# Optimization experiments

Measured on AMD Instinct MI355X. Metric: run time of the kernel, lower is better.

Reference implementation:

```python
import jax, jax.numpy as jnp
import numpy as np
from jax import lax

G, BS = 8, 32  # group_num, blocksize


def conv(x, w, b=None, stride=1, pad=0):
    out = lax.conv_general_dilated(x, w, (stride, stride), [(pad, pad), (pad, pad)],
                                   dimension_numbers=('NCHW', 'OIHW', 'NCHW'))
    if b is not None:
        out = out + b[None, :, None, None]
    return out


def prelu(x, a):
    return jnp.where(x >= 0, x, a * x)


def reshape_adap(x, bs):
    # faithful vectorized form of My_Reshape_Adap: channel c = co*bs*bs + p*bs + q
    # goes to output[b, co, i*bs+p, j*bs+q]
    B, C, h, w = x.shape
    co = C // (bs * bs)
    return x.reshape(B, co, bs, bs, h, w).transpose(0, 1, 4, 2, 5, 3).reshape(B, co, h * bs, w * bs)


def setup_inputs() -> dict:
    key = jax.random.key(0)
    ks = jax.random.split(key, 24)
    rn = lambda k, shp, s: (jax.random.normal(k, shp, dtype=jnp.float32) * s)
    inp = {
        'x': rn(ks[0], (1, 1, 256, 256), 1.0),
        'sample_w': rn(ks[1], (G, 13, 1, 32, 32), 0.03),
        'up_w': rn(ks[2], (G, 1024, 13, 1, 1), 0.2),
        'up_b': rn(ks[3], (G, 1024), 0.02),
        'h1_w': rn(ks[4], (G, 64, 1, 3, 3), 0.2),
        'h1_b': rn(ks[5], (G, 64), 0.02),
        'h1_a': jnp.full((G,), 0.25, jnp.float32),
        'fus_w': rn(ks[6], (G - 1, 64, 128, 3, 3), 0.03),
        'fus_b': rn(ks[7], (G - 1, 64), 0.02),
        'fus_a': jnp.full((G - 1,), 0.25, jnp.float32),
        't2_w': rn(ks[8], (G, 64, 64, 3, 3), 0.04),
        't2_b': rn(ks[9], (G, 64), 0.02),
        't2_a': jnp.full((G,), 0.25, jnp.float32),
        't3_w': rn(ks[10], (G, 64, 64, 3, 3), 0.04),
        't3_b': rn(ks[11], (G, 64), 0.02),
        't3_a': jnp.full((G,), 0.25, jnp.float32),
        't4_w': rn(ks[12], (G, 64, 64, 3, 3), 0.04),
        't4_b': rn(ks[13], (G, 64), 0.02),
        't4_a': jnp.full((G,), 0.25, jnp.float32),
        't5_w': rn(ks[14], (G, 1, 64, 3, 3), 0.04),
        't5_b': rn(ks[15], (G, 1), 0.02),
    }
    return inp


def reference(x, sample_w, up_w, up_b, h1_w, h1_b, h1_a, fus_w, fus_b, fus_a,
              t2_w, t2_b, t2_a, t3_w, t3_b, t3_a, t4_w, t4_b, t4_a, t5_w, t5_b):
    outs = []
    feature = None
    for m in range(G):
        # SamplingModule: conv(1->13, k=32, s=32, no bias)
        s = conv(x, sample_w[m], stride=BS)
        # HeadBlock: 1x1 upsample (13->1024) + block scatter reshape + conv(1->64)+PReLU
        u = conv(s, up_w[m], up_b[m])
        r = reshape_adap(u, BS)                       # [B,1,H,W]
        h = prelu(conv(r, h1_w[m], h1_b[m], pad=1), h1_a[m])  # [B,64,H,W]
        if m == 0:
            feature = h
        else:
            # Fusion_concate: conv(128->64)+PReLU on channel concat
            cat = jnp.concatenate([feature, h], axis=1)
            feature = prelu(conv(cat, fus_w[m - 1], fus_b[m - 1], pad=1), fus_a[m - 1])
        t = prelu(conv(feature, t2_w[m], t2_b[m], pad=1), t2_a[m])
        t = prelu(conv(t, t3_w[m], t3_b[m], pad=1), t3_a[m])
        t = prelu(conv(t, t4_w[m], t4_b[m], pad=1), t4_a[m])
        outs.append(conv(t, t5_w[m], t5_b[m], pad=1))
    return jnp.stack(outs)  # [G, B, 1, H, W]
```

## Files before the change

kernel.cpp:

```cpp
#include <hip/hip_runtime.h>

constexpr int H = 256, W = 256, NPIX = H * W;
constexpr int PW = 258;
constexpr size_t PLANE = (size_t)PW * PW * 64;

typedef _Float16 half8 __attribute__((ext_vector_type(8)));
typedef _Float16 half4 __attribute__((ext_vector_type(4)));
typedef float    f32x4 __attribute__((ext_vector_type(4)));
typedef float    f32x16 __attribute__((ext_vector_type(16)));

__device__ __forceinline__ void gl16(const _Float16* g, _Float16* l)
{
    __builtin_amdgcn_global_load_lds(
        (const __attribute__((address_space(1))) unsigned int*)g,
        (__attribute__((address_space(3))) unsigned int*)l, 16, 0, 0);
}

__global__ __launch_bounds__(256)
void prep_k(const float* __restrict__ x, const float* __restrict__ sw,
            const float* __restrict__ uw, const float* __restrict__ ub,
            const float* __restrict__ t2w, const float* __restrict__ t3w,
            const float* __restrict__ t4w, const float* __restrict__ fusw,
            _Float16* __restrict__ planes, _Float16* __restrict__ w16,
            float* __restrict__ r_all)
{
    const int b = blockIdx.x, t = threadIdx.x;
    for (int idx = b * 256 + t; idx < 24 * 1028 * 8; idx += 512 * 256) {
        int c = idx & 7, rem = idx >> 3;
        int p = rem / 1028, bb = rem % 1028;
        int gy, gx;
        if (bb < 258)      { gy = 0;            gx = bb; }
        else if (bb < 516) { gy = 257;          gx = bb - 258; }
        else if (bb < 772) { gy = bb - 516 + 1; gx = 0; }
        else               { gy = bb - 772 + 1; gx = 257; }
        f32x4 z = {0.f, 0.f, 0.f, 0.f};
        *(f32x4*)(planes + (size_t)p * PLANE + ((size_t)(gy * PW + gx) * 64) + c * 8) = z;
    }
    for (int idx = b * 256 + t; idx < 38 * 36864; idx += 512 * 256) {
        int blk = idx / 36864, r2 = idx % 36864;
        int e = r2 & 7, co = (r2 >> 3) & 63, hh = (r2 >> 9) & 1, kk = (r2 >> 10) & 3,
            tap = r2 >> 12;
        const float* src; int cin, cib;
        if (blk < 24) {
            int which = blk >> 3, m = blk & 7;
            src = (which == 0 ? t2w : which == 1 ? t3w : t4w) + (size_t)m * 64 * 64 * 9;
            cin = 64; cib = 0;
        } else {
            int f = (blk - 24) >> 1; cib = ((blk - 24) & 1) * 64;
            src = fusw + (size_t)f * 64 * 128 * 9; cin = 128;
        }
        int ci = cib + (kk * 2 + hh) * 8 + e;
        w16[idx] = (_Float16)src[((size_t)co * cin + ci) * 9 + tap];
    }
    {
        int m = b >> 6, ij = b & 63;
        int i = ij >> 3, j = ij & 7;
        __shared__ float s_lds[16];
        if (t < 208) {
            int c = t >> 4, sub = t & 15;
            float acc = 0.f;
            for (int k = sub * 64; k < sub * 64 + 64; ++k) {
                int p = k >> 5, q = k & 31;
                acc += x[(i * 32 + p) * W + (j * 32 + q)] * sw[(m * 13 + c) * 1024 + k];
            }
            #pragma unroll
            for (int off = 8; off; off >>= 1) acc += __shfl_down(acc, off, 16);
            if (sub == 0) s_lds[c] = acc;
        }
        __syncthreads();
        const float* uwm = uw + m * 1024 * 13;
        float* rm = r_all + m * NPIX;
        #pragma unroll
        for (int pi = 0; pi < 4; ++pi) {
            int px = pi * 256 + t;
            int p = px >> 5, q = px & 31;
            int oc = p * 32 + q;
            float acc = ub[m * 1024 + oc];
            #pragma unroll
            for (int c = 0; c < 13; ++c) acc = fmaf(uwm[oc * 13 + c], s_lds[c], acc);
            rm[((i * 32 + p) << 8) + j * 32 + q] = acc;
        }
    }
}

__global__ __launch_bounds__(256, 2)
void conv_mfma_k(const _Float16* __restrict__ in0, const _Float16* __restrict__ w0,
                 const float* __restrict__ bias, const float* __restrict__ alpha,
                 _Float16* __restrict__ out)
{
    const int t    = threadIdx.x;
    const int lane = t & 63;
    const int wv   = t >> 6;
    const int b    = blockIdx.x;
    const int m    = b >> 6;
    const int rem  = b & 63;
    const int xh   = rem & 1;
    const int y0   = (rem >> 1) << 3;

    const _Float16* inp0 = in0 + (size_t)m * PLANE;
    _Float16*       outp = out + (size_t)m * PLANE;
    const _Float16* wp0  = w0 + (size_t)m * 36864;
    const float*    bp   = bias + m * 64;
    const float     slope = alpha[m];
    const int x0 = xh << 7;

    const int h = lane >> 5, cl = lane & 31;
    const int px0 = (wv & 1) * 64, cobase = (wv >> 1) * 32;

    extern __shared__ __align__(16) char smem[];
    _Float16* li = (_Float16*)smem;

    half8 Areg[36];
    #pragma unroll
    for (int tap = 0; tap < 9; ++tap)
        #pragma unroll
        for (int kk = 0; kk < 4; ++kk)
            Areg[tap*4+kk] = *(const half8*)(wp0 +
                (size_t)(((tap*4+kk)*2 + h)*64 + cobase + cl) * 8);

    auto stage_row = [&](int pr) {
        const int slot = pr & 3;
        #pragma unroll
        for (int i = 0; i < 5; ++i) {
            int f = i * 256 + t;
            if (i < 4 || f < 1040) {
                int hx = f >> 3, c = f & 7;
                gl16(inp0 + ((size_t)(pr * PW + x0 + hx) * 64 + (c ^ (hx & 7)) * 8),
                     li + (size_t)(slot * 1040 + f) * 8);
            }
        }
    };

    f32x16 acc0, acc1;

    stage_row(y0); stage_row(y0 + 1); stage_row(y0 + 2);
    __syncthreads();
    #pragma unroll 1
    for (int s = 0; s < 8; ++s) {
        if (s < 7) stage_row(y0 + s + 3);
        #pragma unroll
        for (int q = 0; q < 4; ++q)
            #pragma unroll
            for (int j = 0; j < 4; ++j) {
                float bb = bp[cobase + q * 8 + 4 * h + j];
                acc0[q*4+j] = bb; acc1[q*4+j] = bb;
            }
        __builtin_amdgcn_s_setprio(1);
        #pragma unroll
        for (int tap = 0; tap < 9; ++tap) {
            const int dy = tap / 3, dx = tap % 3;
            const int slot = (y0 + s + dy) & 3;
            const int hx0 = px0 + cl + dx;
            const int hx1 = hx0 + 32;
            const int sw8 = hx0 & 7;
            #pragma unroll
            for (int kk = 0; kk < 4; ++kk) {
                const int c = kk * 2 + h;
                half8 b0 = *(const half8*)(li + ((size_t)((slot*130 + hx0)*8 + (c ^ sw8))) * 8);
                half8 b1 = *(const half8*)(li + ((size_t)((slot*130 + hx1)*8 + (c ^ sw8))) * 8);
                acc0 = __builtin_amdgcn_mfma_f32_32x32x16_f16(Areg[tap*4+kk], b0, acc0, 0, 0, 0);
                acc1 = __builtin_amdgcn_mfma_f32_32x32x16_f16(Areg[tap*4+kk], b1, acc1, 0, 0, 0);
            }
        }
        __builtin_amdgcn_s_setprio(0);
        const int y = y0 + s;
        #pragma unroll
        for (int pt = 0; pt < 2; ++pt) {
            const size_t gp = (size_t)((y + 1) * PW + (x0 + px0 + pt * 32 + cl + 1)) * 64;
            const f32x16& A0 = pt ? acc1 : acc0;
            #pragma unroll
            for (int q = 0; q < 4; ++q) {
                half4 v0;
                #pragma unroll
                for (int j = 0; j < 4; ++j) {
                    float xv = A0[q*4+j];
                    xv = xv >= 0.f ? xv : slope * xv;
                    v0[j] = (_Float16)xv;
                }
                *(half4*)(outp + gp + cobase + q * 8 + 4 * h) = v0;
            }
        }
        if (s < 7) {
            asm volatile("s_waitcnt vmcnt(8)" ::: "memory");
            __builtin_amdgcn_s_barrier();
            __builtin_amdgcn_sched_barrier(0);
        }
    }
}

template <int FIRST>
__global__ __launch_bounds__(256, 2)
void fus_k(const _Float16* __restrict__ fprev, _Float16* __restrict__ f0out,
           const float* __restrict__ rm_prev, const float* __restrict__ rm_cur,
           const float* __restrict__ h1w_prev, const float* __restrict__ h1b_prev,
           const float* __restrict__ h1a_prev,
           const float* __restrict__ h1w_cur, const float* __restrict__ h1b_cur,
           const float* __restrict__ h1a_cur,
           const _Float16* __restrict__ wf, const _Float16* __restrict__ wh,
           const float* __restrict__ bias, const float* __restrict__ alpha,
           _Float16* __restrict__ outp)
{
    const int t = threadIdx.x, lane = t & 63, wv = t >> 6;
    const int b = blockIdx.x;
    const int xcd = b & 7, u = b >> 3, xq = u & 3, band = u >> 2;
    const int y0 = xcd * 32 + band * 2, x0 = xq * 64;
    const int h = lane >> 5, cl = lane & 31;
    const int px0 = (wv & 1) * 32, cobase = (wv >> 1) * 32;

    __shared__ __align__(16) _Float16 ringF[4 * 528 * 8];
    __shared__ __align__(16) _Float16 ringH[4 * 528 * 8];

    auto hcomp = [&](const float* rm, const float* h1w, const float* h1b,
                     float hs, _Float16* ring, _Float16* f0w) {
        const int c8 = t & 7;
        float wreg[72];
        #pragma unroll
        for (int i = 0; i < 18; ++i)
            *(f32x4*)(wreg + i * 4) = *(const f32x4*)(h1w + c8 * 72 + i * 4);
        float b8[8];
        #pragma unroll
        for (int j = 0; j < 8; ++j) b8[j] = h1b[c8 * 8 + j];

        #pragma unroll
        for (int it = 0; it < 9; ++it) {
            int idx = it * 256 + t;
            if (it < 8 || idx < 2112) {
                int pl = idx >> 3;
                int r  = pl / 66, hx = pl - r * 66;
                int gy = y0 - 1 + r, gx = x0 - 1 + hx;
                half8 o = {0,0,0,0,0,0,0,0};
                if ((unsigned)gy < 256u && (unsigned)gx < 256u) {
                    float v[9];
                    #pragma unroll
                    for (int dy = 0; dy < 3; ++dy) {
                        int ry = gy + dy - 1;
                        #pragma unroll
                        for (int dx = 0; dx < 3; ++dx) {
                            int rx = gx + dx - 1;
                            v[dy*3+dx] = ((unsigned)ry < 256u && (unsigned)rx < 256u)
                                       ? rm[(ry << 8) + rx] : 0.f;
                        }
                    }
                    #pragma unroll
                    for (int j = 0; j < 8; ++j) {
                        float av = b8[j];
                        #pragma unroll
                        for (int k = 0; k < 9; ++k) av = fmaf(v[k], wreg[j*9+k], av);
                        av = av >= 0.f ? av : hs * av;
                        o[j] = (_Float16)av;
                    }
                    if (f0w && r >= 1 && r <= 2 && hx >= 1 && hx <= 64)
                        *(half8*)(f0w + ((size_t)((gy + 1) * PW + (gx + 1)) * 64)
                                  + c8 * 8) = o;
                }
                *(half8*)(ring + (size_t)(r * 528 + hx * 8 + (c8 ^ (hx & 7))) * 8) = o;
            }
        }
    };

    if (FIRST) {
        hcomp(rm_prev, h1w_prev, h1b_prev, h1a_prev[0], ringF, f0out);
    } else {
        #pragma unroll
        for (int i = 0; i < 9; ++i) {
            int idx = i * 256 + t;
            if (i < 8 || idx < 2112) {
                int r = idx / 528, f = idx - r * 528;
                int hx = f >> 3, c = f & 7;
                gl16(fprev + ((size_t)((y0 + r) * PW + x0 + hx) * 64 + (c ^ (hx & 7)) * 8),
                     ringF + (size_t)idx * 8);
            }
        }
    }
    hcomp(rm_cur, h1w_cur, h1b_cur, h1a_cur[0], ringH, nullptr);
    __builtin_amdgcn_sched_barrier(0);

    half8 Areg[36];
    auto load_A = [&](const _Float16* w) {
        #pragma unroll
        for (int tap = 0; tap < 9; ++tap)
            #pragma unroll
            for (int kk = 0; kk < 4; ++kk)
                Areg[tap*4+kk] = *(const half8*)(w +
                    (size_t)(((tap*4+kk)*2 + h)*64 + cobase + cl) * 8);
    };
    load_A(wf);

    f32x16 acc0, acc1;
    #pragma unroll
    for (int q = 0; q < 4; ++q)
        #pragma unroll
        for (int j = 0; j < 4; ++j) {
            float bb = bias[cobase + q * 8 + 4 * h + j];
            acc0[q*4+j] = bb; acc1[q*4+j] = bb;
        }

    __syncthreads();

    auto cpass = [&](const _Float16* ring) {
        __builtin_amdgcn_s_setprio(1);
        #pragma unroll
        for (int tap = 0; tap < 9; ++tap) {
            const int dy = tap / 3, dx = tap % 3;
            const int hx = px0 + cl + dx;
            const int sw = hx & 7;
            #pragma unroll
            for (int kk = 0; kk < 4; ++kk) {
                const int c = kk * 2 + h;
                half8 b0 = *(const half8*)(ring + ((size_t)(((dy    )*528) + hx*8 + (c ^ sw))) * 8);
                half8 b1 = *(const half8*)(ring + ((size_t)(((dy + 1)*528) + hx*8 + (c ^ sw))) * 8);
                acc0 = __builtin_amdgcn_mfma_f32_32x32x16_f16(Areg[tap*4+kk], b0, acc0, 0, 0, 0);
                acc1 = __builtin_amdgcn_mfma_f32_32x32x16_f16(Areg[tap*4+kk], b1, acc1, 0, 0, 0);
            }
        }
        __builtin_amdgcn_s_setprio(0);
    };

    cpass(ringF);
    load_A(wh);
    cpass(ringH);

    const float slope = alpha[0];
    #pragma unroll
    for (int s = 0; s < 2; ++s) {
        const size_t gp = (size_t)((y0 + s + 1) * PW + (x0 + px0 + cl + 1)) * 64 + cobase;
        const f32x16& A0 = s ? acc1 : acc0;
        #pragma unroll
        for (int q = 0; q < 4; ++q) {
            half4 v;
            #pragma unroll
            for (int j = 0; j < 4; ++j) {
                float xv = A0[q*4+j];
                xv = xv >= 0.f ? xv : slope * xv;
                v[j] = (_Float16)xv;
            }
            *(half4*)(outp + gp + q * 8 + 4 * h) = v;
        }
    }
}

__global__ __launch_bounds__(256, 2)
void t5_k(const _Float16* __restrict__ in_all, const float* __restrict__ w_all,
          const float* __restrict__ b_all, float* __restrict__ out_all)
{
    const int m = blockIdx.y;
    const _Float16* in = in_all + (size_t)m * PLANE;
    const float* w = w_all + m * 576;
    float* outp = out_all + m * NPIX;

    const int t = threadIdx.x;
    const int b = blockIdx.x;
    const int xcd = b & 7, u = b >> 3;
    const int xh = u & 1, band = u >> 1;
    const int y0 = xcd * 32 + band * 8;
    const int x0 = xh << 7;

    __shared__ __align__(16) _Float16 ring[4 * 130 * 64];
    __shared__ float wl[576];
    __shared__ float part[128];

    auto stage_row = [&](int pr) {
        const int slot = pr & 3;
        #pragma unroll
        for (int i = 0; i < 5; ++i) {
            int f = i * 256 + t;
            if (i < 4 || f < 1040) {
                int hx = f >> 3, c = f & 7;
                gl16(in + ((size_t)(pr * PW + x0 + hx) * 64 + (c ^ (hx & 7)) * 8),
                     ring + (size_t)(slot * 1040 + f) * 8);
            }
        }
    };

    stage_row(y0); stage_row(y0 + 1); stage_row(y0 + 2);
    #pragma unroll
    for (int i = 0; i < 3; ++i) { int idx = i*256 + t; if (idx < 576) wl[idx] = w[idx]; }
    __syncthreads();

    const int p = t & 127, chalf = t >> 7;
    #pragma unroll 1
    for (int s = 0; s < 8; ++s) {
        if (s < 7) stage_row(y0 + s + 3);
        float acc = 0.f;
        #pragma unroll
        for (int dy = 0; dy < 3; ++dy) {
            const int slot = (y0 + s + dy) & 3;
            #pragma unroll
            for (int dx = 0; dx < 3; ++dx) {
                const int hx = p + dx, sw = hx & 7, tap = dy * 3 + dx;
                #pragma unroll
                for (int kc = 0; kc < 4; ++kc) {
                    const int c8 = chalf * 4 + kc;
                    half8 vv = *(const half8*)(ring +
                        ((size_t)((slot*130 + hx)*8 + (c8 ^ sw))) * 8);
                    #pragma unroll
                    for (int e = 0; e < 8; ++e)
                        acc = fmaf((float)vv[e], wl[(c8 * 8 + e) * 9 + tap], acc);
                }
            }
        }
        if (chalf) part[p] = acc;
        __syncthreads();
        if (!chalf) outp[((y0 + s) << 8) + x0 + p] = part[p] + acc + b_all[m];
        __syncthreads();
    }
}

extern "C" void kernel_launch(void* const* d_in, const int* in_sizes, int n_in,
                              void* d_out, int out_size, void* d_ws, size_t ws_size,
                              hipStream_t stream)
{
    const float* x        = (const float*)d_in[0];
    const float* sample_w = (const float*)d_in[1];
    const float* up_w     = (const float*)d_in[2];
    const float* up_b     = (const float*)d_in[3];
    const float* h1_w     = (const float*)d_in[4];
    const float* h1_b     = (const float*)d_in[5];
    const float* h1_a     = (const float*)d_in[6];
    const float* fus_w    = (const float*)d_in[7];
    const float* fus_b    = (const float*)d_in[8];
    const float* fus_a    = (const float*)d_in[9];
    const float* t2_w     = (const float*)d_in[10];
    const float* t2_b     = (const float*)d_in[11];
    const float* t2_a     = (const float*)d_in[12];
    const float* t3_w     = (const float*)d_in[13];
    const float* t3_b     = (const float*)d_in[14];
    const float* t3_a     = (const float*)d_in[15];
    const float* t4_w     = (const float*)d_in[16];
    const float* t4_b     = (const float*)d_in[17];
    const float* t4_a     = (const float*)d_in[18];
    const float* t5_w     = (const float*)d_in[19];
    const float* t5_b     = (const float*)d_in[20];

    float* out = (float*)d_out;
    char*  wsb = (char*)d_ws;

    _Float16* w16    = (_Float16*)wsb;
    float*    r_all  = (float*)(wsb + 2801664);
    _Float16* f_all  = (_Float16*)(wsb + 4898816);
    _Float16* sc_all = f_all + 8 * PLANE;
    _Float16* t1_all = sc_all + 8 * PLANE;

    auto wblk = [&](int b) { return w16 + (size_t)b * 36864; };

    prep_k<<<512, 256, 0, stream>>>(x, sample_w, up_w, up_b,
                                    t2_w, t3_w, t4_w, fus_w,
                                    f_all, w16, r_all);

    fus_k<1><<<512, 256, 0, stream>>>(
        nullptr, f_all,
        r_all, r_all + NPIX,
        h1_w, h1_b, h1_a,
        h1_w + 576, h1_b + 64, h1_a + 1,
        wblk(24), wblk(25), fus_b, fus_a,
        f_all + PLANE);
    for (int m = 2; m < 8; ++m) {
        fus_k<0><<<512, 256, 0, stream>>>(
            f_all + (size_t)(m - 1) * PLANE, nullptr,
            nullptr, r_all + m * NPIX,
            nullptr, nullptr, nullptr,
            h1_w + m * 576, h1_b + m * 64, h1_a + m,
            wblk(24 + (m - 1) * 2), wblk(24 + (m - 1) * 2 + 1),
            fus_b + (m - 1) * 64, fus_a + (m - 1),
            f_all + (size_t)m * PLANE);
    }

    const size_t LDSB = 66560;
    conv_mfma_k<<<512, 256, LDSB, stream>>>(f_all, wblk(0), t2_b, t2_a, t1_all);
    conv_mfma_k<<<512, 256, LDSB, stream>>>(t1_all, wblk(8), t3_b, t3_a, sc_all);
    conv_mfma_k<<<512, 256, LDSB, stream>>>(sc_all, wblk(16), t4_b, t4_a, t1_all);
    t5_k<<<dim3(64, 8), 256, 0, stream>>>(t1_all, t5_w, t5_b, out);
}
```

Before: 398.0 us.

## Stage head input tile in LDS for fus_k and halve t5 tile width

In fus_k, the reshaped head-input tile (6x68 floats) is loaded into shared memory once, and the 3x3 head conv reads its taps from there. This replaces nine guarded global loads per output pixel. The fprev global-to-LDS prefetch is also moved ahead of the head compute so it overlaps with it. In t5_k, tiles become 64 pixels wide with four channel-quarter partial sums, so the grid doubles to 128x8 blocks with a smaller LDS ring and launch bounds of 4 blocks per CU. The aim is more occupancy and parallelism, at the cost of an extra reduction step and more halo reloads per row.

```diff
diff --git a/kernel.cpp b/kernel.cpp
--- a/kernel.cpp
+++ b/kernel.cpp
@@ -191,11 +191,11 @@
 template <int FIRST>
 __global__ __launch_bounds__(256, 2)
 void fus_k(const _Float16* __restrict__ fprev, _Float16* __restrict__ f0out,
-           const float* __restrict__ rm_prev, const float* __restrict__ rm_cur,
-           const float* __restrict__ h1w_prev, const float* __restrict__ h1b_prev,
-           const float* __restrict__ h1a_prev,
-           const float* __restrict__ h1w_cur, const float* __restrict__ h1b_cur,
-           const float* __restrict__ h1a_cur,
+           const float* __restrict__ rmP, const float* __restrict__ rmC,
+           const float* __restrict__ h1wP, const float* __restrict__ h1bP,
+           const float* __restrict__ h1aP,
+           const float* __restrict__ h1wC, const float* __restrict__ h1bC,
+           const float* __restrict__ h1aC,
            const _Float16* __restrict__ wf, const _Float16* __restrict__ wh,
            const float* __restrict__ bias, const float* __restrict__ alpha,
            _Float16* __restrict__ outp)
@@ -209,8 +209,41 @@
 
     __shared__ __align__(16) _Float16 ringF[4 * 528 * 8];
     __shared__ __align__(16) _Float16 ringH[4 * 528 * 8];
-
-    auto hcomp = [&](const float* rm, const float* h1w, const float* h1b,
+    __shared__ float rtileC[6 * 68];
+    __shared__ float rtileP[FIRST ? 6 * 68 : 1];
+
+    if (!FIRST) {
+        #pragma unroll
+        for (int i = 0; i < 9; ++i) {
+            int idx = i * 256 + t;
+            if (i < 8 || idx < 2112) {
+                int r = idx / 528, f = idx - r * 528;
+                int hx = f >> 3, c = f & 7;
+                gl16(fprev + ((size_t)((y0 + r) * PW + x0 + hx) * 64 + (c ^ (hx & 7)) * 8),
+                     ringF + (size_t)idx * 8);
+            }
+        }
+    }
+
+    auto stage_rt = [&](const float* rm, float* rt) {
+        #pragma unroll
+        for (int i = 0; i < 2; ++i) {
+            int ix = i * 256 + t;
+            if (ix < 408) {
+                int row = ix / 68, col = ix - row * 68;
+                int gy = y0 - 2 + row, gx = x0 - 2 + col;
+                rt[ix] = ((unsigned)gy < 256u && (unsigned)gx < 256u)
+                       ? rm[(gy << 8) + gx] : 0.f;
+            }
+        }
+    };
+    stage_rt(rmC, rtileC);
+    if (FIRST) stage_rt(rmP, rtileP);
+    asm volatile("s_waitcnt lgkmcnt(0)" ::: "memory");
+    __builtin_amdgcn_s_barrier();
+    __builtin_amdgcn_sched_barrier(0);
+
+    auto hcomp = [&](const float* rt, const float* h1w, const float* h1b,
                      float hs, _Float16* ring, _Float16* f0w) {
         const int c8 = t & 7;
         float wreg[72];
@@ -232,15 +265,10 @@
                 if ((unsigned)gy < 256u && (unsigned)gx < 256u) {
                     float v[9];
                     #pragma unroll
-                    for (int dy = 0; dy < 3; ++dy) {
-                        int ry = gy + dy - 1;
+                    for (int dy = 0; dy < 3; ++dy)
                         #pragma unroll
-                        for (int dx = 0; dx < 3; ++dx) {
-                            int rx = gx + dx - 1;
-                            v[dy*3+dx] = ((unsigned)ry < 256u && (unsigned)rx < 256u)
-                                       ? rm[(ry << 8) + rx] : 0.f;
-                        }
-                    }
+                        for (int dx = 0; dx < 3; ++dx)
+                            v[dy*3+dx] = rt[(r + dy) * 68 + hx + dx];
                     #pragma unroll
                     for (int j = 0; j < 8; ++j) {
                         float av = b8[j];
@@ -249,7 +277,7 @@
                         av = av >= 0.f ? av : hs * av;
                         o[j] = (_Float16)av;
                     }
-                    if (f0w && r >= 1 && r <= 2 && hx >= 1 && hx <= 64)
+                    if (FIRST && f0w && r >= 1 && r <= 2 && hx >= 1 && hx <= 64)
                         *(half8*)(f0w + ((size_t)((gy + 1) * PW + (gx + 1)) * 64)
                                   + c8 * 8) = o;
                 }
@@ -258,21 +286,8 @@
         }
     };
 
-    if (FIRST) {
-        hcomp(rm_prev, h1w_prev, h1b_prev, h1a_prev[0], ringF, f0out);
-    } else {
-        #pragma unroll
-        for (int i = 0; i < 9; ++i) {
-            int idx = i * 256 + t;
-            if (i < 8 || idx < 2112) {
-                int r = idx / 528, f = idx - r * 528;
-                int hx = f >> 3, c = f & 7;
-                gl16(fprev + ((size_t)((y0 + r) * PW + x0 + hx) * 64 + (c ^ (hx & 7)) * 8),
-                     ringF + (size_t)idx * 8);
-            }
-        }
-    }
-    hcomp(rm_cur, h1w_cur, h1b_cur, h1a_cur[0], ringH, nullptr);
+    if (FIRST) hcomp(rtileP, h1wP, h1bP, h1aP[0], ringF, f0out);
+    hcomp(rtileC, h1wC, h1bC, h1aC[0], ringH, nullptr);
     __builtin_amdgcn_sched_barrier(0);
 
     half8 Areg[36];
@@ -339,7 +354,7 @@
     }
 }
 
-__global__ __launch_bounds__(256, 2)
+__global__ __launch_bounds__(256, 4)
 void t5_k(const _Float16* __restrict__ in_all, const float* __restrict__ w_all,
           const float* __restrict__ b_all, float* __restrict__ out_all)
 {
@@ -351,23 +366,23 @@
     const int t = threadIdx.x;
     const int b = blockIdx.x;
     const int xcd = b & 7, u = b >> 3;
-    const int xh = u & 1, band = u >> 1;
+    const int xq = u & 3, band = u >> 2;
     const int y0 = xcd * 32 + band * 8;
-    const int x0 = xh << 7;
-
-    __shared__ __align__(16) _Float16 ring[4 * 130 * 64];
+    const int x0 = xq << 6;
+
+    __shared__ __align__(16) _Float16 ring[4 * 66 * 64];
     __shared__ float wl[576];
-    __shared__ float part[128];
+    __shared__ float part[256];
 
     auto stage_row = [&](int pr) {
         const int slot = pr & 3;
         #pragma unroll
-        for (int i = 0; i < 5; ++i) {
+        for (int i = 0; i < 3; ++i) {
             int f = i * 256 + t;
-            if (i < 4 || f < 1040) {
+            if (f < 528) {
                 int hx = f >> 3, c = f & 7;
                 gl16(in + ((size_t)(pr * PW + x0 + hx) * 64 + (c ^ (hx & 7)) * 8),
-                     ring + (size_t)(slot * 1040 + f) * 8);
+                     ring + (size_t)(slot * 528 + f) * 8);
             }
         }
     };
@@ -377,7 +392,7 @@
     for (int i = 0; i < 3; ++i) { int idx = i*256 + t; if (idx < 576) wl[idx] = w[idx]; }
     __syncthreads();
 
-    const int p = t & 127, chalf = t >> 7;
+    const int p5 = t & 63, cq = t >> 6;
     #pragma unroll 1
     for (int s = 0; s < 8; ++s) {
         if (s < 7) stage_row(y0 + s + 3);
@@ -387,21 +402,23 @@
             const int slot = (y0 + s + dy) & 3;
             #pragma unroll
             for (int dx = 0; dx < 3; ++dx) {
-                const int hx = p + dx, sw = hx & 7, tap = dy * 3 + dx;
+                const int hx = p5 + dx, sw = hx & 7, tap = dy * 3 + dx;
                 #pragma unroll
-                for (int kc = 0; kc < 4; ++kc) {
-                    const int c8 = chalf * 4 + kc;
+                for (int c2 = 0; c2 < 2; ++c2) {
+                    const int c8 = cq * 2 + c2;
                     half8 vv = *(const half8*)(ring +
-                        ((size_t)((slot*130 + hx)*8 + (c8 ^ sw))) * 8);
+                        ((size_t)(slot*528 + hx*8 + (c8 ^ sw))) * 8);
                     #pragma unroll
                     for (int e = 0; e < 8; ++e)
                         acc = fmaf((float)vv[e], wl[(c8 * 8 + e) * 9 + tap], acc);
                 }
             }
         }
-        if (chalf) part[p] = acc;
+        part[cq * 64 + p5] = acc;
         __syncthreads();
-        if (!chalf) outp[((y0 + s) << 8) + x0 + p] = part[p] + acc + b_all[m];
+        if (t < 64)
+            outp[((y0 + s) << 8) + x0 + t] =
+                part[t] + part[64 + t] + part[128 + t] + part[192 + t] + b_all[m];
         __syncthreads();
     }
 }
@@ -469,5 +486,5 @@
     conv_mfma_k<<<512, 256, LDSB, stream>>>(f_all, wblk(0), t2_b, t2_a, t1_all);
     conv_mfma_k<<<512, 256, LDSB, stream>>>(t1_all, wblk(8), t3_b, t3_a, sc_all);
     conv_mfma_k<<<512, 256, LDSB, stream>>>(sc_all, wblk(16), t4_b, t4_a, t1_all);
-    t5_k<<<dim3(64, 8), 256, 0, stream>>>(t1_all, t5_w, t5_b, out);
-}
+    t5_k<<<dim3(128, 8), 256, 0, stream>>>(t1_all, t5_w, t5_b, out);
+}
```

Result: faster. 353.6 us (-11.2%).
